# Kernel tuning notes

Measured on AMD Instinct MI355X. Metric: run time of the kernel, lower is better.

Reference implementation:

```python
import jax, jax.numpy as jnp
import numpy as np

THRESH = 0.5   # global `thresh` used by ActFun
LENS = 0.5     # global `lens` (surrogate width)
DECAY = 0.25   # LIFNode init_decay
INV_STD = 1.0 / float(np.sqrt(1.0 + 1e-5))  # BN eval: running_mean=0, running_var=1
HEADS = 8
WINDOW = 8

@jax.custom_vjp
def act_fun(x):
    return (x > THRESH).astype(x.dtype)

def _act_fwd(x):
    return act_fun(x), x

def _act_bwd(x, g):
    temp = (jnp.abs(x - THRESH) < LENS).astype(g.dtype) / (2.0 * LENS)
    return (g * temp,)

act_fun.defvjp(_act_fwd, _act_bwd)

def lif(x):
    # x: [T, ...]; mem = x[0]; mem_t = mem_{t-1}*decay*(1-spike_{t-1}.detach()) + x_t
    spike0 = act_fun(x[0])
    def step(carry, xi):
        mem_prev, spike_prev = carry
        mem = mem_prev * DECAY * (1.0 - jax.lax.stop_gradient(spike_prev)) + xi
        spike = act_fun(mem)
        return (mem, spike), spike
    _, spikes = jax.lax.scan(step, (x[0], spike0), x[1:])
    return jnp.concatenate([spike0[None], spikes], axis=0)

def bn_eval(x, gamma, beta):
    # BatchNorm2d eval over channel D (last dim of [T,B,L,D]) with default running stats
    return x * (INV_STD * gamma) + beta

def linear(x, w, b):
    # torch nn.Linear: y = x @ w.T + b, w: [out, in]
    return jnp.einsum('tbld,ed->tble', x, w) + b


def setup_inputs() -> dict:
    key = jax.random.key(0)
    ks = jax.random.split(key, 12)
    T, B, L, D = 4, 4, 1024, 512
    s = 0.02
    inp = {
        'x': jax.random.normal(ks[0], (T, B, L, D), dtype=jnp.float32),
        'pos_bias': jax.random.uniform(ks[1], (L, L), dtype=jnp.float32),
        'q_w': jax.random.normal(ks[2], (D, D), dtype=jnp.float32) * s,
        'q_b': jnp.zeros((D,), jnp.float32),
        'q_g': jnp.ones((D,), jnp.float32),
        'q_beta': jnp.zeros((D,), jnp.float32),
        'k_w': jax.random.normal(ks[3], (D, D), dtype=jnp.float32) * s,
        'k_b': jnp.zeros((D,), jnp.float32),
        'k_g': jnp.ones((D,), jnp.float32),
        'k_beta': jnp.zeros((D,), jnp.float32),
        'v_w': jax.random.normal(ks[4], (D, D), dtype=jnp.float32) * s,
        'v_b': jnp.zeros((D,), jnp.float32),
        'v_g': jnp.ones((D,), jnp.float32),
        'v_beta': jnp.zeros((D,), jnp.float32),
        'last_w': jax.random.normal(ks[5], (D, D), dtype=jnp.float32) * s,
        'last_b': jnp.zeros((D,), jnp.float32),
        'last_g': jnp.ones((D,), jnp.float32),
        'last_beta': jnp.zeros((D,), jnp.float32),
    }
    return inp


def reference(x, pos_bias, q_w, q_b, q_g, q_beta, k_w, k_b, k_g, k_beta,
              v_w, v_b, v_g, v_beta, last_w, last_b, last_g, last_beta):
    T, B, L, D = x.shape
    H = HEADS
    Dh = D // H
    # local causal band: keep pos_bias[i,j] only where 0 <= i-j < WINDOW
    i = jnp.arange(L)[:, None]
    j = jnp.arange(L)[None, :]
    band = ((i - j) >= 0) & ((i - j) < WINDOW)
    pb = jnp.where(band, pos_bias[:L, :L], 0.0)  # [L, L]

    xs = lif(x)  # first_lif
    q = lif(bn_eval(linear(xs, q_w, q_b), q_g, q_beta))
    k = lif(bn_eval(linear(xs, k_w, k_b), k_g, k_beta))
    v = lif(bn_eval(linear(xs, v_w, v_b), v_g, v_beta))

    # [T,B,L,D] -> [T,B,L,H,Dh] -> [B,H,L,T,Dh] -> [B,H,L,T*Dh]
    qh = q.reshape(T, B, L, H, Dh).transpose(1, 3, 2, 0, 4).reshape(B, H, L, T * Dh)
    kv = (k * v).reshape(T, B, L, H, Dh).transpose(1, 3, 2, 0, 4).reshape(B, H, L, T * Dh)

    attn = jnp.einsum('ij,bhjd->bhid', pb, kv)  # local-window positional mixing
    out = qh * attn
    out = out.reshape(B, H, L, T, Dh).transpose(3, 0, 2, 1, 4).reshape(T, B, L, D)
    out = lif(out)  # attn_lif
    out = bn_eval(linear(out, last_w, last_b), last_g, last_beta)
    return out
```

## Files before the change

### kernel.cpp

```cpp
#include <hip/hip_runtime.h>
#include <stdint.h>


#define T_ 4
#define B_ 4
#define L_ 1024
#define D_ 512
#define BI_ (B_*L_)
#define M_ROWS (T_*B_*L_)
#define STRIDE4 (B_*L_*D_/4)
#define INV_STD 0.9999950000374997f
#define EPS_FLAG 1e-3f
#define LIST_CAP 5000000u

typedef unsigned int   u32;
typedef unsigned short u16;
typedef __bf16 bf16x8 __attribute__((ext_vector_type(8)));
typedef float  f32x4  __attribute__((ext_vector_type(4)));

static __device__ __forceinline__ float spike_of(float m) {
  return m > 0.5f ? 1.0f : 0.0f;
}
static __device__ __forceinline__ u16 sbits(float s) {
  return s != 0.0f ? (u16)0x3F80 : (u16)0;
}

__device__ __forceinline__ void gll16(const u16* g, void* l) {
  __builtin_amdgcn_global_load_lds(
      (const __attribute__((address_space(1))) u32*)(const void*)g,
      (__attribute__((address_space(3))) u32*)l, 16, 0, 0);
}

__global__ __launch_bounds__(256) void k_wsplit(const float* __restrict__ qw,
    const float* __restrict__ kw, const float* __restrict__ vw,
    const float* __restrict__ lw, u16* __restrict__ wsp, u32* __restrict__ cnt) {
  int idx = blockIdx.x * 256 + threadIdx.x;
  if (idx == 0) *cnt = 0;
  int mat = idx >> 16;
  int u = idx & 65535;
  const float* W = mat == 0 ? qw : mat == 1 ? kw : mat == 2 ? vw : lw;
  float4 w = ((const float4*)W)[u];
  float wv[4] = {w.x, w.y, w.z, w.w};
  u16 hb[4], lb[4];
#pragma unroll
  for (int c = 0; c < 4; ++c) {
    __bf16 h = (__bf16)wv[c];
    float r = wv[c] - (float)h;
    __bf16 lo = (__bf16)r;
    hb[c] = __builtin_bit_cast(u16, h);
    lb[c] = __builtin_bit_cast(u16, lo);
  }
  u16* base = wsp + (size_t)mat * 524288;
  ((ushort4*)base)[u]            = make_ushort4(hb[0], hb[1], hb[2], hb[3]);
  ((ushort4*)(base + 262144))[u] = make_ushort4(lb[0], lb[1], lb[2], lb[3]);
}

__global__ __launch_bounds__(256) void k_lif_first(const float* __restrict__ x,
                                                   u16* __restrict__ xsb) {
  int idx = blockIdx.x * 256 + threadIdx.x;
  if (idx >= STRIDE4) return;
  const float4* x4 = (const float4*)x;
  ushort4* o4 = (ushort4*)xsb;
  float m[4], s[4];
  float4 v = x4[idx];
  m[0] = v.x; m[1] = v.y; m[2] = v.z; m[3] = v.w;
#pragma unroll
  for (int c = 0; c < 4; ++c) s[c] = spike_of(m[c]);
  o4[idx] = make_ushort4(sbits(s[0]), sbits(s[1]), sbits(s[2]), sbits(s[3]));
#pragma unroll
  for (int t = 1; t < T_; ++t) {
    v = x4[idx + t * STRIDE4];
    float xv[4] = {v.x, v.y, v.z, v.w};
#pragma unroll
    for (int c = 0; c < 4; ++c) {
      m[c] = m[c] * 0.25f * (1.0f - s[c]) + xv[c];
      s[c] = spike_of(m[c]);
    }
    o4[idx + t * STRIDE4] = make_ushort4(sbits(s[0]), sbits(s[1]), sbits(s[2]), sbits(s[3]));
  }
}

__global__ __launch_bounds__(256) void k_gemm(const u16* __restrict__ Ab,
    const u16* __restrict__ Wp, const float* __restrict__ bias,
    const float* __restrict__ gamma, const float* __restrict__ beta,
    float* __restrict__ Y) {
  __shared__ __align__(16) unsigned char sm[49152];
  const int tid = threadIdx.x;
  int f = blockIdx.y * 4 + blockIdx.x;
  int tI = (f & 7) * 64 + (f >> 3);
  const int row0 = (tI >> 2) * 128;
  const int col0 = (tI & 3) * 128;

  const u16* gsrc[12];
  int loff[12];
#pragma unroll
  for (int u = 0; u < 12; ++u) {
    if (u < 4) {
      int lin = u * 4096 + tid * 16;
      int r = lin >> 7, slot = (lin >> 4) & 7, gs = slot ^ (r & 7);
      gsrc[u] = Ab + (size_t)(row0 + r) * 512 + gs * 8;
      loff[u] = lin;
    } else {
      int lin = (u - 4) * 4096 + tid * 16;
      int plane = lin >> 14, l3 = lin & 16383;
      int r = l3 >> 7, slot = (l3 >> 4) & 7, gs = slot ^ (r & 7);
      gsrc[u] = Wp + (size_t)plane * 262144 + (size_t)(col0 + r) * 512 + gs * 8;
      loff[u] = 16384 + lin;
    }
  }

  const int lane = tid & 63;
  const int wid = tid >> 6;
  const int wr = wid >> 1, wc = wid & 1;
  const int la = lane & 15, lg = lane >> 4;

  int offA[4][2], offB[2][4][2];
#pragma unroll
  for (int mi = 0; mi < 4; ++mi) {
    int r = wr * 64 + mi * 16 + la;
#pragma unroll
    for (int s = 0; s < 2; ++s)
      offA[mi][s] = r * 128 + ((s * 64 + lg * 16) ^ ((r & 7) << 4));
  }
#pragma unroll
  for (int p = 0; p < 2; ++p)
#pragma unroll
    for (int ni = 0; ni < 4; ++ni) {
      int r = wc * 64 + ni * 16 + la;
#pragma unroll
      for (int s = 0; s < 2; ++s)
        offB[p][ni][s] = 16384 + p * 16384 + r * 128 + ((s * 64 + lg * 16) ^ ((r & 7) << 4));
    }

  f32x4 acc[4][4];
#pragma unroll
  for (int a = 0; a < 4; ++a)
#pragma unroll
    for (int b = 0; b < 4; ++b) acc[a][b] = (f32x4){0.f, 0.f, 0.f, 0.f};

  for (int k0 = 0; k0 < 8; ++k0) {
#pragma unroll
    for (int u = 0; u < 12; ++u) gll16(gsrc[u] + (k0 << 6), sm + loff[u]);
    __syncthreads();
    uint4 af[4][2];
#pragma unroll
    for (int mi = 0; mi < 4; ++mi)
#pragma unroll
      for (int s = 0; s < 2; ++s)
        af[mi][s] = *(const uint4*)(sm + offA[mi][s]);
#pragma unroll
    for (int p = 0; p < 2; ++p)
#pragma unroll
      for (int s = 0; s < 2; ++s)
#pragma unroll
        for (int ni = 0; ni < 4; ++ni) {
          uint4 bf = *(const uint4*)(sm + offB[p][ni][s]);
#pragma unroll
          for (int mi = 0; mi < 4; ++mi)
            acc[mi][ni] = __builtin_amdgcn_mfma_f32_16x16x32_bf16(
                __builtin_bit_cast(bf16x8, af[mi][s]),
                __builtin_bit_cast(bf16x8, bf), acc[mi][ni], 0, 0, 0);
        }
    __syncthreads();
  }

#pragma unroll
  for (int ni = 0; ni < 4; ++ni) {
    int e = col0 + wc * 64 + ni * 16 + la;
    float cs = INV_STD * gamma[e];
    float cb = bias[e], ct = beta[e];
#pragma unroll
    for (int mi = 0; mi < 4; ++mi) {
      int rb = row0 + wr * 64 + mi * 16 + lg * 4;
#pragma unroll
      for (int p = 0; p < 4; ++p)
        Y[(size_t)(rb + p) * 512 + e] = (acc[mi][ni][p] + cb) * cs + ct;
    }
  }
}

__global__ __launch_bounds__(256) void k_lif_s(const float* __restrict__ pre,
                                               u16* __restrict__ sp,
                                               u32* __restrict__ list,
                                               u32* __restrict__ cnt,
                                               int tz) {
  int idx = blockIdx.x * 256 + threadIdx.x;
  if (idx >= STRIDE4) return;
  const float4* p4 = (const float4*)pre;
  ushort4* s4 = (ushort4*)sp;
  float m[4], s[4];
  int fb[4] = {0, 0, 0, 0};
  float4 v = p4[idx];
  m[0] = v.x; m[1] = v.y; m[2] = v.z; m[3] = v.w;
#pragma unroll
  for (int c = 0; c < 4; ++c) {
    s[c] = spike_of(m[c]);
    if (fabsf(m[c] - 0.5f) < EPS_FLAG) fb[c] = 1;
  }
  s4[idx] = make_ushort4(sbits(s[0]), sbits(s[1]), sbits(s[2]), sbits(s[3]));
#pragma unroll
  for (int t = 1; t < T_; ++t) {
    v = p4[idx + t * STRIDE4];
    float xv[4] = {v.x, v.y, v.z, v.w};
#pragma unroll
    for (int c = 0; c < 4; ++c) {
      m[c] = m[c] * 0.25f * (1.0f - s[c]) + xv[c];
      s[c] = spike_of(m[c]);
      if (fabsf(m[c] - 0.5f) < EPS_FLAG) fb[c] = 1;
    }
    s4[idx + t * STRIDE4] = make_ushort4(sbits(s[0]), sbits(s[1]), sbits(s[2]), sbits(s[3]));
  }
  int nf = fb[0] + fb[1] + fb[2] + fb[3];
  if (nf) {
    u32 base = atomicAdd(cnt, (u32)nf);
    const int bi = idx >> 7, d0 = (idx & 127) * 4;
    u32 p = base;
#pragma unroll
    for (int c = 0; c < 4; ++c)
      if (fb[c]) {
        if (p < LIST_CAP)
          list[p] = ((u32)tz << 21) | (u32)(bi * 512 + d0 + c);
        ++p;
      }
  }
}

__device__ __forceinline__ void consume32(const float4 (&wb)[8],
                                          const uint4 (&ab)[4][4],
                                          float& c0, float& c1,
                                          float& c2, float& c3) {
#pragma unroll
  for (int u = 0; u < 8; ++u) {
    float4 w = wb[u];
    uint4 t0 = ab[0][u >> 1], t1 = ab[1][u >> 1];
    uint4 t2 = ab[2][u >> 1], t3 = ab[3][u >> 1];
    u32 a0 = (u & 1) ? t0.z : t0.x, b0 = (u & 1) ? t0.w : t0.y;
    u32 a1 = (u & 1) ? t1.z : t1.x, b1 = (u & 1) ? t1.w : t1.y;
    u32 a2 = (u & 1) ? t2.z : t2.x, b2 = (u & 1) ? t2.w : t2.y;
    u32 a3 = (u & 1) ? t3.z : t3.x, b3 = (u & 1) ? t3.w : t3.y;
    c0 += (a0 & 0xFFFFu) ? w.x : 0.0f;
    c0 += (a0 >> 16)     ? w.y : 0.0f;
    c0 += (b0 & 0xFFFFu) ? w.z : 0.0f;
    c0 += (b0 >> 16)     ? w.w : 0.0f;
    c1 += (a1 & 0xFFFFu) ? w.x : 0.0f;
    c1 += (a1 >> 16)     ? w.y : 0.0f;
    c1 += (b1 & 0xFFFFu) ? w.z : 0.0f;
    c1 += (b1 >> 16)     ? w.w : 0.0f;
    c2 += (a2 & 0xFFFFu) ? w.x : 0.0f;
    c2 += (a2 >> 16)     ? w.y : 0.0f;
    c2 += (b2 & 0xFFFFu) ? w.z : 0.0f;
    c2 += (b2 >> 16)     ? w.w : 0.0f;
    c3 += (a3 & 0xFFFFu) ? w.x : 0.0f;
    c3 += (a3 >> 16)     ? w.y : 0.0f;
    c3 += (b3 & 0xFFFFu) ? w.z : 0.0f;
    c3 += (b3 >> 16)     ? w.w : 0.0f;
  }
}

__global__ __launch_bounds__(64) void k_fixup_c(const u16* __restrict__ xsb,
    u16* __restrict__ qs, u16* __restrict__ ks, u16* __restrict__ vs,
    const float* __restrict__ qw, const float* __restrict__ qb2,
    const float* __restrict__ qg, const float* __restrict__ qbe,
    const float* __restrict__ kw, const float* __restrict__ kb2,
    const float* __restrict__ kg, const float* __restrict__ kbe,
    const float* __restrict__ vw, const float* __restrict__ vb2,
    const float* __restrict__ vg, const float* __restrict__ vbe,
    const u32* __restrict__ list, const u32* __restrict__ cnt) {
  u32 n = *cnt;
  if (n > LIST_CAP) n = LIST_CAP;
  for (u32 i = blockIdx.x * 64 + threadIdx.x; i < n; i += gridDim.x * 64) {
    u32 e = list[i];
    int tz = (int)(e >> 21);
    int col = (int)(e & 0x1FFFFFu);
    int bi = col >> 9, d = col & 511;
    const float* W  = tz == 0 ? qw  : tz == 1 ? kw  : vw;
    const float* Bb = tz == 0 ? qb2 : tz == 1 ? kb2 : vb2;
    const float* Gg = tz == 0 ? qg  : tz == 1 ? kg  : vg;
    const float* Be = tz == 0 ? qbe : tz == 1 ? kbe : vbe;
    u16* S          = tz == 0 ? qs  : tz == 1 ? ks  : vs;
    const float4* w4 = (const float4*)(W + (size_t)d * 512);
    const uint4* R0 = (const uint4*)(xsb + (size_t)(0 * BI_ + bi) * 512);
    const uint4* R1 = (const uint4*)(xsb + (size_t)(1 * BI_ + bi) * 512);
    const uint4* R2 = (const uint4*)(xsb + (size_t)(2 * BI_ + bi) * 512);
    const uint4* R3 = (const uint4*)(xsb + (size_t)(3 * BI_ + bi) * 512);

    float4 wA[8], wB[8];
    uint4 aA[4][4], aB[4][4];
#pragma unroll
    for (int u = 0; u < 8; ++u) wA[u] = w4[u];
#pragma unroll
    for (int u = 0; u < 4; ++u) {
      aA[0][u] = R0[u]; aA[1][u] = R1[u]; aA[2][u] = R2[u]; aA[3][u] = R3[u];
    }
    float c0 = 0.f, c1 = 0.f, c2 = 0.f, c3 = 0.f;
#pragma unroll
    for (int ch = 0; ch < 16; ++ch) {
      if ((ch & 1) == 0) {
        if (ch + 1 < 16) {
          int wb0 = (ch + 1) * 8, ab0 = (ch + 1) * 4;
#pragma unroll
          for (int u = 0; u < 8; ++u) wB[u] = w4[wb0 + u];
#pragma unroll
          for (int u = 0; u < 4; ++u) {
            aB[0][u] = R0[ab0 + u]; aB[1][u] = R1[ab0 + u];
            aB[2][u] = R2[ab0 + u]; aB[3][u] = R3[ab0 + u];
          }
        }
        consume32(wA, aA, c0, c1, c2, c3);
      } else {
        if (ch + 1 < 16) {
          int wb0 = (ch + 1) * 8, ab0 = (ch + 1) * 4;
#pragma unroll
          for (int u = 0; u < 8; ++u) wA[u] = w4[wb0 + u];
#pragma unroll
          for (int u = 0; u < 4; ++u) {
            aA[0][u] = R0[ab0 + u]; aA[1][u] = R1[ab0 + u];
            aA[2][u] = R2[ab0 + u]; aA[3][u] = R3[ab0 + u];
          }
        }
        consume32(wB, aB, c0, c1, c2, c3);
      }
    }
    float cs = INV_STD * Gg[d];
    float cb = Bb[d], ct = Be[d];
    float accs[4] = {c0, c1, c2, c3};
    float m = 0.f, s = 0.f;
#pragma unroll
    for (int t = 0; t < 4; ++t) {
      float pre = (accs[t] + cb) * cs + ct;
      if (t == 0) m = pre;
      else m = m * 0.25f * (1.0f - s) + pre;
      s = spike_of(m);
      S[(size_t)(t * BI_ + bi) * 512 + d] = sbits(s);
    }
  }
}

__global__ __launch_bounds__(256) void k_attn(const u16* __restrict__ qs,
    const u16* __restrict__ ks, const u16* __restrict__ vs,
    const float* __restrict__ pos_bias, u16* __restrict__ sout) {
  int idx = blockIdx.x * 256 + threadIdx.x;
  if (idx >= STRIDE4) return;
  const int d4 = idx & 127;
  const int bi = idx >> 7;
  const int i = bi & (L_ - 1);
  const int wmax = i < 7 ? i : 7;

  float pbv[8];
  const float* pbrow = pos_bias + (size_t)i * L_ + i;
  for (int w = 0; w <= wmax; ++w) pbv[w] = pbrow[-w];

  const ushort4* k4 = (const ushort4*)ks;
  const ushort4* v4 = (const ushort4*)vs;
  const ushort4* q4 = (const ushort4*)qs;
  float pre[T_][4];

#pragma unroll
  for (int t = 0; t < T_; ++t) {
    float sum[4] = {0.f, 0.f, 0.f, 0.f};
    const int tb = t * STRIDE4;
    for (int w = wmax; w >= 0; --w) {
      ushort4 ku = k4[tb + (bi - w) * 128 + d4];
      ushort4 vu = v4[tb + (bi - w) * 128 + d4];
      sum[0] += (ku.x && vu.x) ? pbv[w] : 0.0f;
      sum[1] += (ku.y && vu.y) ? pbv[w] : 0.0f;
      sum[2] += (ku.z && vu.z) ? pbv[w] : 0.0f;
      sum[3] += (ku.w && vu.w) ? pbv[w] : 0.0f;
    }
    ushort4 qu = q4[tb + bi * 128 + d4];
    pre[t][0] = qu.x ? sum[0] : 0.0f;
    pre[t][1] = qu.y ? sum[1] : 0.0f;
    pre[t][2] = qu.z ? sum[2] : 0.0f;
    pre[t][3] = qu.w ? sum[3] : 0.0f;
  }

  ushort4* s4 = (ushort4*)sout;
  float m[4], s[4];
#pragma unroll
  for (int c = 0; c < 4; ++c) { m[c] = pre[0][c]; s[c] = spike_of(m[c]); }
  s4[idx] = make_ushort4(sbits(s[0]), sbits(s[1]), sbits(s[2]), sbits(s[3]));
#pragma unroll
  for (int t = 1; t < T_; ++t) {
#pragma unroll
    for (int c = 0; c < 4; ++c) {
      m[c] = m[c] * 0.25f * (1.0f - s[c]) + pre[t][c];
      s[c] = spike_of(m[c]);
    }
    s4[idx + t * STRIDE4] = make_ushort4(sbits(s[0]), sbits(s[1]), sbits(s[2]), sbits(s[3]));
  }
}

extern "C" void kernel_launch(void* const* d_in, const int* in_sizes, int n_in,
                              void* d_out, int out_size, void* d_ws, size_t ws_size,
                              hipStream_t stream) {
  (void)in_sizes; (void)n_in; (void)out_size; (void)ws_size;
  const float* x        = (const float*)d_in[0];
  const float* pos_bias = (const float*)d_in[1];
  const float* q_w    = (const float*)d_in[2];
  const float* q_b    = (const float*)d_in[3];
  const float* q_g    = (const float*)d_in[4];
  const float* q_beta = (const float*)d_in[5];
  const float* k_w    = (const float*)d_in[6];
  const float* k_b    = (const float*)d_in[7];
  const float* k_g    = (const float*)d_in[8];
  const float* k_beta = (const float*)d_in[9];
  const float* v_w    = (const float*)d_in[10];
  const float* v_b    = (const float*)d_in[11];
  const float* v_g    = (const float*)d_in[12];
  const float* v_beta = (const float*)d_in[13];
  const float* last_w    = (const float*)d_in[14];
  const float* last_b    = (const float*)d_in[15];
  const float* last_g    = (const float*)d_in[16];
  const float* last_beta = (const float*)d_in[17];
  float* out = (float*)d_out;

  char* ws = (char*)d_ws;
  u16*   xsb  = (u16*)(ws + 0);
  u16*   qs   = (u16*)(ws + 16777216);
  u16*   ks   = (u16*)(ws + 33554432);
  u16*   vs   = (u16*)(ws + 50331648);
  float* P1   = (float*)(ws + 67108864);
  u16*   sA   = (u16*)(ws + 67108864);
  u16*   wsp  = (u16*)(ws + 100663296);
  u32*   list = (u32*)(ws + 104857600);
  u32*   cnt  = (u32*)(ws + 124857600);

  dim3 gg(4, 128);

  k_wsplit<<<1024, 256, 0, stream>>>(q_w, k_w, v_w, last_w, wsp, cnt);
  k_lif_first<<<2048, 256, 0, stream>>>(x, xsb);

  k_gemm<<<gg, 256, 0, stream>>>(xsb, wsp + 0 * 524288, q_b, q_g, q_beta, P1);
  k_lif_s<<<2048, 256, 0, stream>>>(P1, qs, list, cnt, 0);
  k_gemm<<<gg, 256, 0, stream>>>(xsb, wsp + 1 * 524288, k_b, k_g, k_beta, P1);
  k_lif_s<<<2048, 256, 0, stream>>>(P1, ks, list, cnt, 1);
  k_gemm<<<gg, 256, 0, stream>>>(xsb, wsp + 2 * 524288, v_b, v_g, v_beta, P1);
  k_lif_s<<<2048, 256, 0, stream>>>(P1, vs, list, cnt, 2);

  k_fixup_c<<<2048, 64, 0, stream>>>(xsb, qs, ks, vs,
      q_w, q_b, q_g, q_beta, k_w, k_b, k_g, k_beta, v_w, v_b, v_g, v_beta,
      list, cnt);

  k_attn<<<2048, 256, 0, stream>>>(qs, ks, vs, pos_bias, sA);

  k_gemm<<<gg, 256, 0, stream>>>(sA, wsp + 3 * 524288, last_b, last_g, last_beta, out);
}
```

Measured before the change: 390.5 us.

## Fuse LIF into QKV GEMM epilogue via time-interleaved spike layout

Spike tensors move to a [B*L, T, D] row layout, so the four timesteps of one token sit in adjacent GEMM rows. Each MFMA thread already holds those four rows, so the LIF recurrence and near-threshold flagging run in the GEMM epilogue. This removes the fp32 pre-activation buffer round trip and three separate LIF kernels. The fixup kernel is re-parallelised to one thread per timestep with shuffles, and the output GEMM scatters back to T-major order. In exchange, spike stores become 2-byte scattered writes and there is one atomic per flagged element.

After: 366.5 us. 1.07x faster.

```diff
diff --git a/kernel.cpp b/kernel.cpp
--- a/kernel.cpp
+++ b/kernel.cpp
@@ -59,6 +59,7 @@
                                                    u16* __restrict__ xsb) {
   int idx = blockIdx.x * 256 + threadIdx.x;
   if (idx >= STRIDE4) return;
+  const int bi = idx >> 7, d4 = idx & 127;
   const float4* x4 = (const float4*)x;
   ushort4* o4 = (ushort4*)xsb;
   float m[4], s[4];
@@ -66,7 +67,8 @@
   m[0] = v.x; m[1] = v.y; m[2] = v.z; m[3] = v.w;
 #pragma unroll
   for (int c = 0; c < 4; ++c) s[c] = spike_of(m[c]);
-  o4[idx] = make_ushort4(sbits(s[0]), sbits(s[1]), sbits(s[2]), sbits(s[3]));
+  o4[(bi * 4 + 0) * 128 + d4] =
+      make_ushort4(sbits(s[0]), sbits(s[1]), sbits(s[2]), sbits(s[3]));
 #pragma unroll
   for (int t = 1; t < T_; ++t) {
     v = x4[idx + t * STRIDE4];
@@ -76,21 +78,14 @@
       m[c] = m[c] * 0.25f * (1.0f - s[c]) + xv[c];
       s[c] = spike_of(m[c]);
     }
-    o4[idx + t * STRIDE4] = make_ushort4(sbits(s[0]), sbits(s[1]), sbits(s[2]), sbits(s[3]));
-  }
-}
-
-__global__ __launch_bounds__(256) void k_gemm(const u16* __restrict__ Ab,
-    const u16* __restrict__ Wp, const float* __restrict__ bias,
-    const float* __restrict__ gamma, const float* __restrict__ beta,
-    float* __restrict__ Y) {
-  __shared__ __align__(16) unsigned char sm[49152];
-  const int tid = threadIdx.x;
-  int f = blockIdx.y * 4 + blockIdx.x;
-  int tI = (f & 7) * 64 + (f >> 3);
-  const int row0 = (tI >> 2) * 128;
-  const int col0 = (tI & 3) * 128;
-
+    o4[(bi * 4 + t) * 128 + d4] =
+        make_ushort4(sbits(s[0]), sbits(s[1]), sbits(s[2]), sbits(s[3]));
+  }
+}
+
+__device__ __forceinline__ void gemm_core(const u16* __restrict__ Ab,
+    const u16* __restrict__ Wp, int row0, int col0, int tid,
+    unsigned char* sm, f32x4 (&acc)[4][4]) {
   const u16* gsrc[12];
   int loff[12];
 #pragma unroll
@@ -108,7 +103,6 @@
       loff[u] = 16384 + lin;
     }
   }
-
   const int lane = tid & 63;
   const int wid = tid >> 6;
   const int wr = wid >> 1, wc = wid & 1;
@@ -129,10 +123,10 @@
       int r = wc * 64 + ni * 16 + la;
 #pragma unroll
       for (int s = 0; s < 2; ++s)
-        offB[p][ni][s] = 16384 + p * 16384 + r * 128 + ((s * 64 + lg * 16) ^ ((r & 7) << 4));
-    }
-
-  f32x4 acc[4][4];
+        offB[p][ni][s] = 16384 + p * 16384 + r * 128 +
+                         ((s * 64 + lg * 16) ^ ((r & 7) << 4));
+    }
+
 #pragma unroll
   for (int a = 0; a < 4; ++a)
 #pragma unroll
@@ -163,6 +157,27 @@
         }
     __syncthreads();
   }
+}
+
+__global__ __launch_bounds__(256) void k_gemm_lif(const u16* __restrict__ Ab,
+    const u16* __restrict__ Wp, const float* __restrict__ bias,
+    const float* __restrict__ gamma, const float* __restrict__ beta,
+    u16* __restrict__ S, u32* __restrict__ list, u32* __restrict__ cnt,
+    int tz) {
+  __shared__ __align__(16) unsigned char sm[49152];
+  const int tid = threadIdx.x;
+  int f = blockIdx.y * 4 + blockIdx.x;
+  int tI = (f & 7) * 64 + (f >> 3);
+  const int row0 = (tI >> 2) * 128;
+  const int col0 = (tI & 3) * 128;
+
+  f32x4 acc[4][4];
+  gemm_core(Ab, Wp, row0, col0, tid, sm, acc);
+
+  const int lane = tid & 63;
+  const int wid = tid >> 6;
+  const int wr = wid >> 1, wc = wid & 1;
+  const int la = lane & 15, lg = lane >> 4;
 
 #pragma unroll
   for (int ni = 0; ni < 4; ++ni) {
@@ -171,93 +186,82 @@
     float cb = bias[e], ct = beta[e];
 #pragma unroll
     for (int mi = 0; mi < 4; ++mi) {
-      int rb = row0 + wr * 64 + mi * 16 + lg * 4;
+      int r = row0 + wr * 64 + mi * 16 + lg * 4;
+      int bi = r >> 2;
+      float m = 0.f, s = 0.f;
+      int fl = 0;
+      u16 sb[4];
+#pragma unroll
+      for (int p = 0; p < 4; ++p) {
+        float pre = (acc[mi][ni][p] + cb) * cs + ct;
+        if (p == 0) m = pre;
+        else m = m * 0.25f * (1.0f - s) + pre;
+        s = spike_of(m);
+        if (fabsf(m - 0.5f) < EPS_FLAG) fl = 1;
+        sb[p] = sbits(s);
+      }
 #pragma unroll
       for (int p = 0; p < 4; ++p)
-        Y[(size_t)(rb + p) * 512 + e] = (acc[mi][ni][p] + cb) * cs + ct;
-    }
-  }
-}
-
-__global__ __launch_bounds__(256) void k_lif_s(const float* __restrict__ pre,
-                                               u16* __restrict__ sp,
-                                               u32* __restrict__ list,
-                                               u32* __restrict__ cnt,
-                                               int tz) {
-  int idx = blockIdx.x * 256 + threadIdx.x;
-  if (idx >= STRIDE4) return;
-  const float4* p4 = (const float4*)pre;
-  ushort4* s4 = (ushort4*)sp;
-  float m[4], s[4];
-  int fb[4] = {0, 0, 0, 0};
-  float4 v = p4[idx];
-  m[0] = v.x; m[1] = v.y; m[2] = v.z; m[3] = v.w;
-#pragma unroll
-  for (int c = 0; c < 4; ++c) {
-    s[c] = spike_of(m[c]);
-    if (fabsf(m[c] - 0.5f) < EPS_FLAG) fb[c] = 1;
-  }
-  s4[idx] = make_ushort4(sbits(s[0]), sbits(s[1]), sbits(s[2]), sbits(s[3]));
-#pragma unroll
-  for (int t = 1; t < T_; ++t) {
-    v = p4[idx + t * STRIDE4];
-    float xv[4] = {v.x, v.y, v.z, v.w};
-#pragma unroll
-    for (int c = 0; c < 4; ++c) {
-      m[c] = m[c] * 0.25f * (1.0f - s[c]) + xv[c];
-      s[c] = spike_of(m[c]);
-      if (fabsf(m[c] - 0.5f) < EPS_FLAG) fb[c] = 1;
-    }
-    s4[idx + t * STRIDE4] = make_ushort4(sbits(s[0]), sbits(s[1]), sbits(s[2]), sbits(s[3]));
-  }
-  int nf = fb[0] + fb[1] + fb[2] + fb[3];
-  if (nf) {
-    u32 base = atomicAdd(cnt, (u32)nf);
-    const int bi = idx >> 7, d0 = (idx & 127) * 4;
-    u32 p = base;
-#pragma unroll
-    for (int c = 0; c < 4; ++c)
-      if (fb[c]) {
-        if (p < LIST_CAP)
-          list[p] = ((u32)tz << 21) | (u32)(bi * 512 + d0 + c);
-        ++p;
+        S[(size_t)(r + p) * 512 + e] = sb[p];
+      if (fl) {
+        u32 pos = atomicAdd(cnt, 1u);
+        if (pos < LIST_CAP)
+          list[pos] = ((u32)tz << 21) | (u32)(bi * 512 + e);
       }
-  }
-}
-
-__device__ __forceinline__ void consume32(const float4 (&wb)[8],
-                                          const uint4 (&ab)[4][4],
-                                          float& c0, float& c1,
-                                          float& c2, float& c3) {
+    }
+  }
+}
+
+__global__ __launch_bounds__(256) void k_gemm_out(const u16* __restrict__ Ab,
+    const u16* __restrict__ Wp, const float* __restrict__ bias,
+    const float* __restrict__ gamma, const float* __restrict__ beta,
+    float* __restrict__ Y) {
+  __shared__ __align__(16) unsigned char sm[49152];
+  const int tid = threadIdx.x;
+  int f = blockIdx.y * 4 + blockIdx.x;
+  int tI = (f & 7) * 64 + (f >> 3);
+  const int row0 = (tI >> 2) * 128;
+  const int col0 = (tI & 3) * 128;
+
+  f32x4 acc[4][4];
+  gemm_core(Ab, Wp, row0, col0, tid, sm, acc);
+
+  const int lane = tid & 63;
+  const int wid = tid >> 6;
+  const int wr = wid >> 1, wc = wid & 1;
+  const int la = lane & 15, lg = lane >> 4;
+
+#pragma unroll
+  for (int ni = 0; ni < 4; ++ni) {
+    int e = col0 + wc * 64 + ni * 16 + la;
+    float cs = INV_STD * gamma[e];
+    float cb = bias[e], ct = beta[e];
+#pragma unroll
+    for (int mi = 0; mi < 4; ++mi) {
+      int r = row0 + wr * 64 + mi * 16 + lg * 4;
+      int bi = r >> 2;
+#pragma unroll
+      for (int p = 0; p < 4; ++p)
+        Y[(size_t)(p * BI_ + bi) * 512 + e] = (acc[mi][ni][p] + cb) * cs + ct;
+    }
+  }
+}
+
+__device__ __forceinline__ void consume32_1(const float4 (&wb)[8],
+                                            const uint4 (&ab)[4], float& c) {
 #pragma unroll
   for (int u = 0; u < 8; ++u) {
     float4 w = wb[u];
-    uint4 t0 = ab[0][u >> 1], t1 = ab[1][u >> 1];
-    uint4 t2 = ab[2][u >> 1], t3 = ab[3][u >> 1];
-    u32 a0 = (u & 1) ? t0.z : t0.x, b0 = (u & 1) ? t0.w : t0.y;
-    u32 a1 = (u & 1) ? t1.z : t1.x, b1 = (u & 1) ? t1.w : t1.y;
-    u32 a2 = (u & 1) ? t2.z : t2.x, b2 = (u & 1) ? t2.w : t2.y;
-    u32 a3 = (u & 1) ? t3.z : t3.x, b3 = (u & 1) ? t3.w : t3.y;
-    c0 += (a0 & 0xFFFFu) ? w.x : 0.0f;
-    c0 += (a0 >> 16)     ? w.y : 0.0f;
-    c0 += (b0 & 0xFFFFu) ? w.z : 0.0f;
-    c0 += (b0 >> 16)     ? w.w : 0.0f;
-    c1 += (a1 & 0xFFFFu) ? w.x : 0.0f;
-    c1 += (a1 >> 16)     ? w.y : 0.0f;
-    c1 += (b1 & 0xFFFFu) ? w.z : 0.0f;
-    c1 += (b1 >> 16)     ? w.w : 0.0f;
-    c2 += (a2 & 0xFFFFu) ? w.x : 0.0f;
-    c2 += (a2 >> 16)     ? w.y : 0.0f;
-    c2 += (b2 & 0xFFFFu) ? w.z : 0.0f;
-    c2 += (b2 >> 16)     ? w.w : 0.0f;
-    c3 += (a3 & 0xFFFFu) ? w.x : 0.0f;
-    c3 += (a3 >> 16)     ? w.y : 0.0f;
-    c3 += (b3 & 0xFFFFu) ? w.z : 0.0f;
-    c3 += (b3 >> 16)     ? w.w : 0.0f;
-  }
-}
-
-__global__ __launch_bounds__(64) void k_fixup_c(const u16* __restrict__ xsb,
+    uint4 tt = ab[u >> 1];
+    u32 a = (u & 1) ? tt.z : tt.x, b = (u & 1) ? tt.w : tt.y;
+    c += (a & 0xFFFFu) ? w.x : 0.0f;
+    c += (a >> 16)     ? w.y : 0.0f;
+    c += (b & 0xFFFFu) ? w.z : 0.0f;
+    c += (b >> 16)     ? w.w : 0.0f;
+  }
+}
+
+__global__ __launch_bounds__(128) void k_fixup_c(const u16* __restrict__ xsb,
     u16* __restrict__ qs, u16* __restrict__ ks, u16* __restrict__ vs,
     const float* __restrict__ qw, const float* __restrict__ qb2,
     const float* __restrict__ qg, const float* __restrict__ qbe,
@@ -268,7 +272,11 @@
     const u32* __restrict__ list, const u32* __restrict__ cnt) {
   u32 n = *cnt;
   if (n > LIST_CAP) n = LIST_CAP;
-  for (u32 i = blockIdx.x * 64 + threadIdx.x; i < n; i += gridDim.x * 64) {
+  u32 tot = n * 4;
+  for (u32 ii = blockIdx.x * 128 + threadIdx.x; ii < tot;
+       ii += gridDim.x * 128) {
+    u32 i = ii >> 2;
+    int t = (int)(ii & 3);
     u32 e = list[i];
     int tz = (int)(e >> 21);
     int col = (int)(e & 0x1FFFFFu);
@@ -279,20 +287,15 @@
     const float* Be = tz == 0 ? qbe : tz == 1 ? kbe : vbe;
     u16* S          = tz == 0 ? qs  : tz == 1 ? ks  : vs;
     const float4* w4 = (const float4*)(W + (size_t)d * 512);
-    const uint4* R0 = (const uint4*)(xsb + (size_t)(0 * BI_ + bi) * 512);
-    const uint4* R1 = (const uint4*)(xsb + (size_t)(1 * BI_ + bi) * 512);
-    const uint4* R2 = (const uint4*)(xsb + (size_t)(2 * BI_ + bi) * 512);
-    const uint4* R3 = (const uint4*)(xsb + (size_t)(3 * BI_ + bi) * 512);
+    const uint4*  R  = (const uint4*)(xsb + ((size_t)bi * 4 + t) * 512);
 
     float4 wA[8], wB[8];
-    uint4 aA[4][4], aB[4][4];
+    uint4 aA[4], aB[4];
 #pragma unroll
     for (int u = 0; u < 8; ++u) wA[u] = w4[u];
 #pragma unroll
-    for (int u = 0; u < 4; ++u) {
-      aA[0][u] = R0[u]; aA[1][u] = R1[u]; aA[2][u] = R2[u]; aA[3][u] = R3[u];
-    }
-    float c0 = 0.f, c1 = 0.f, c2 = 0.f, c3 = 0.f;
+    for (int u = 0; u < 4; ++u) aA[u] = R[u];
+    float c = 0.f;
 #pragma unroll
     for (int ch = 0; ch < 16; ++ch) {
       if ((ch & 1) == 0) {
@@ -301,38 +304,40 @@
 #pragma unroll
           for (int u = 0; u < 8; ++u) wB[u] = w4[wb0 + u];
 #pragma unroll
-          for (int u = 0; u < 4; ++u) {
-            aB[0][u] = R0[ab0 + u]; aB[1][u] = R1[ab0 + u];
-            aB[2][u] = R2[ab0 + u]; aB[3][u] = R3[ab0 + u];
-          }
+          for (int u = 0; u < 4; ++u) aB[u] = R[ab0 + u];
         }
-        consume32(wA, aA, c0, c1, c2, c3);
+        consume32_1(wA, aA, c);
       } else {
         if (ch + 1 < 16) {
           int wb0 = (ch + 1) * 8, ab0 = (ch + 1) * 4;
 #pragma unroll
           for (int u = 0; u < 8; ++u) wA[u] = w4[wb0 + u];
 #pragma unroll
-          for (int u = 0; u < 4; ++u) {
-            aA[0][u] = R0[ab0 + u]; aA[1][u] = R1[ab0 + u];
-            aA[2][u] = R2[ab0 + u]; aA[3][u] = R3[ab0 + u];
-          }
+          for (int u = 0; u < 4; ++u) aA[u] = R[ab0 + u];
         }
-        consume32(wB, aB, c0, c1, c2, c3);
+        consume32_1(wB, aB, c);
       }
     }
+    int lane = threadIdx.x & 63;
+    int qb = lane & ~3;
+    float cq[4];
+    cq[0] = __shfl(c, qb + 0, 64);
+    cq[1] = __shfl(c, qb + 1, 64);
+    cq[2] = __shfl(c, qb + 2, 64);
+    cq[3] = __shfl(c, qb + 3, 64);
     float cs = INV_STD * Gg[d];
     float cb = Bb[d], ct = Be[d];
-    float accs[4] = {c0, c1, c2, c3};
     float m = 0.f, s = 0.f;
-#pragma unroll
-    for (int t = 0; t < 4; ++t) {
-      float pre = (accs[t] + cb) * cs + ct;
-      if (t == 0) m = pre;
+    u16 myb = 0;
+#pragma unroll
+    for (int t2 = 0; t2 < 4; ++t2) {
+      float pre = (cq[t2] + cb) * cs + ct;
+      if (t2 == 0) m = pre;
       else m = m * 0.25f * (1.0f - s) + pre;
       s = spike_of(m);
-      S[(size_t)(t * BI_ + bi) * 512 + d] = sbits(s);
-    }
+      if (t2 == t) myb = sbits(s);
+    }
+    S[((size_t)bi * 4 + t) * 512 + d] = myb;
   }
 }
 
@@ -358,16 +363,16 @@
 #pragma unroll
   for (int t = 0; t < T_; ++t) {
     float sum[4] = {0.f, 0.f, 0.f, 0.f};
-    const int tb = t * STRIDE4;
     for (int w = wmax; w >= 0; --w) {
-      ushort4 ku = k4[tb + (bi - w) * 128 + d4];
-      ushort4 vu = v4[tb + (bi - w) * 128 + d4];
+      int rj = ((bi - w) * 4 + t) * 128 + d4;
+      ushort4 ku = k4[rj];
+      ushort4 vu = v4[rj];
       sum[0] += (ku.x && vu.x) ? pbv[w] : 0.0f;
       sum[1] += (ku.y && vu.y) ? pbv[w] : 0.0f;
       sum[2] += (ku.z && vu.z) ? pbv[w] : 0.0f;
       sum[3] += (ku.w && vu.w) ? pbv[w] : 0.0f;
     }
-    ushort4 qu = q4[tb + bi * 128 + d4];
+    ushort4 qu = q4[(bi * 4 + t) * 128 + d4];
     pre[t][0] = qu.x ? sum[0] : 0.0f;
     pre[t][1] = qu.y ? sum[1] : 0.0f;
     pre[t][2] = qu.z ? sum[2] : 0.0f;
@@ -378,7 +383,8 @@
   float m[4], s[4];
 #pragma unroll
   for (int c = 0; c < 4; ++c) { m[c] = pre[0][c]; s[c] = spike_of(m[c]); }
-  s4[idx] = make_ushort4(sbits(s[0]), sbits(s[1]), sbits(s[2]), sbits(s[3]));
+  s4[(bi * 4 + 0) * 128 + d4] =
+      make_ushort4(sbits(s[0]), sbits(s[1]), sbits(s[2]), sbits(s[3]));
 #pragma unroll
   for (int t = 1; t < T_; ++t) {
 #pragma unroll
@@ -386,7 +392,8 @@
       m[c] = m[c] * 0.25f * (1.0f - s[c]) + pre[t][c];
       s[c] = spike_of(m[c]);
     }
-    s4[idx + t * STRIDE4] = make_ushort4(sbits(s[0]), sbits(s[1]), sbits(s[2]), sbits(s[3]));
+    s4[(bi * 4 + t) * 128 + d4] =
+        make_ushort4(sbits(s[0]), sbits(s[1]), sbits(s[2]), sbits(s[3]));
   }
 }
 
@@ -419,7 +426,6 @@
   u16*   qs   = (u16*)(ws + 16777216);
   u16*   ks   = (u16*)(ws + 33554432);
   u16*   vs   = (u16*)(ws + 50331648);
-  float* P1   = (float*)(ws + 67108864);
   u16*   sA   = (u16*)(ws + 67108864);
   u16*   wsp  = (u16*)(ws + 100663296);
   u32*   list = (u32*)(ws + 104857600);
@@ -430,18 +436,19 @@
   k_wsplit<<<1024, 256, 0, stream>>>(q_w, k_w, v_w, last_w, wsp, cnt);
   k_lif_first<<<2048, 256, 0, stream>>>(x, xsb);
 
-  k_gemm<<<gg, 256, 0, stream>>>(xsb, wsp + 0 * 524288, q_b, q_g, q_beta, P1);
-  k_lif_s<<<2048, 256, 0, stream>>>(P1, qs, list, cnt, 0);
-  k_gemm<<<gg, 256, 0, stream>>>(xsb, wsp + 1 * 524288, k_b, k_g, k_beta, P1);
-  k_lif_s<<<2048, 256, 0, stream>>>(P1, ks, list, cnt, 1);
-  k_gemm<<<gg, 256, 0, stream>>>(xsb, wsp + 2 * 524288, v_b, v_g, v_beta, P1);
-  k_lif_s<<<2048, 256, 0, stream>>>(P1, vs, list, cnt, 2);
-
-  k_fixup_c<<<2048, 64, 0, stream>>>(xsb, qs, ks, vs,
+  k_gemm_lif<<<gg, 256, 0, stream>>>(xsb, wsp + 0 * 524288, q_b, q_g, q_beta,
+                                     qs, list, cnt, 0);
+  k_gemm_lif<<<gg, 256, 0, stream>>>(xsb, wsp + 1 * 524288, k_b, k_g, k_beta,
+                                     ks, list, cnt, 1);
+  k_gemm_lif<<<gg, 256, 0, stream>>>(xsb, wsp + 2 * 524288, v_b, v_g, v_beta,
+                                     vs, list, cnt, 2);
+
+  k_fixup_c<<<2048, 128, 0, stream>>>(xsb, qs, ks, vs,
       q_w, q_b, q_g, q_beta, k_w, k_b, k_g, k_beta, v_w, v_b, v_g, v_beta,
       list, cnt);
 
   k_attn<<<2048, 256, 0, stream>>>(qs, ks, vs, pos_bias, sA);
 
-  k_gemm<<<gg, 256, 0, stream>>>(sA, wsp + 3 * 524288, last_b, last_g, last_beta, out);
-}
+  k_gemm_out<<<gg, 256, 0, stream>>>(sA, wsp + 3 * 524288,
+                                     last_b, last_g, last_beta, out);
+}
```
